# Kernel tuning notes

Measured on AMD Instinct MI355X. Metric: run time of the kernel, lower is better.

Reference implementation:

```python
import jax, jax.numpy as jnp
import numpy as np

K_VALUES = (2, 4, 8)  # sorted k_values from init


def setup_inputs() -> dict:
    key = jax.random.key(0)
    ks = jax.random.split(key, 6)
    B, T, D, H = 16, 2048, 512, 64
    nk = len(K_VALUES)
    # columns: (E, Pt, eta, phi) -- E,Pt positive, eta in [-3,3], phi in [-pi,pi]
    u = jax.random.uniform(ks[0], (B, T, 4), jnp.float32)
    tokens_cont = u * jnp.array([100.0, 50.0, 6.0, 6.2832], jnp.float32) + jnp.array([1.0, 1.0, -3.0, -3.1416], jnp.float32)
    lengths = jax.random.randint(ks[1], (B,), T // 2, T + 1)
    mask = jnp.arange(T)[None, :] < lengths[:, None]  # [B,T] True=valid
    W1 = jax.random.normal(ks[2], (nk, H), jnp.float32) / np.sqrt(nk).astype(np.float32)
    b1 = jax.random.normal(ks[3], (H,), jnp.float32) * 0.01
    W2 = jax.random.normal(ks[4], (H, D), jnp.float32) / np.sqrt(H).astype(np.float32)
    b2 = jax.random.normal(ks[5], (D,), jnp.float32) * 0.01
    return dict(tokens_cont=tokens_cont, mask=mask, W1=W1, b1=b1, W2=W2, b2=b2)


def reference(tokens_cont, mask, W1, b1, W2, b2):
    B, T, _ = tokens_cont.shape
    E, Pt, eta, phi = (tokens_cont[..., i] for i in range(4))
    px = Pt * jnp.cos(phi)
    py = Pt * jnp.sin(phi)
    pz = Pt * jnp.sinh(jnp.clip(eta, -20.0, 20.0))
    P = jnp.stack([E, px, py, pz], axis=-1)  # [B,T,4] four-momentum
    metric = jnp.array([1.0, -1.0, -1.0, -1.0], P.dtype)
    # Lorentz dot: E_i E_j - px_i px_j - py_i py_j - pz_i pz_j -> [B,T,T]
    dot = jnp.einsum('btc,bsc->bts', P * metric, P)
    dot = jnp.where(mask[:, None, :], dot, -jnp.inf)  # exclude padding friends
    max_k = min(max(K_VALUES), T)
    _, topk_idx = jax.lax.top_k(dot, max_k)  # [B,T,max_k]
    Pf = P[jnp.arange(B)[:, None, None], topk_idx]  # gather friends [B,T,max_k,4]
    cum = jnp.cumsum(Pf, axis=2)  # prefix sums over sorted friends
    masses = []
    maskf = mask.astype(P.dtype)
    for k in K_VALUES:
        ps = cum[:, :, min(k, max_k) - 1, :]  # [B,T,4] summed 4-momentum of top-k group
        m2 = ps[..., 0] ** 2 - jnp.sum(ps[..., 1:] ** 2, axis=-1)
        m2 = jnp.maximum(m2, 0.0) * maskf
        masses.append(jnp.sqrt(m2 + 1e-8))
    mass = jnp.stack(masses, axis=-1)  # [B,T,n_k]
    h = jax.nn.gelu(mass @ W1 + b1, approximate=False)  # torch GELU = exact erf
    return h @ W2 + b2  # [B,T,model_dim]
```

## Files before the change

kernel.cpp:

```cpp
#include <hip/hip_runtime.h>
#include <hip/hip_bf16.h>
#include <math.h>

#define NB 16
#define NT 2048
#define ND 512
#define NH 64

typedef __attribute__((ext_vector_type(8))) short short8;
typedef __attribute__((ext_vector_type(4))) float float4v;

__device__ __forceinline__ bool mask_is_bytes(const int* m) {
    return m[0] == 0x01010101;
}
__device__ __forceinline__ bool mask_at(const int* m, bool bytes, int i) {
    if (bytes) return ((const unsigned char*)m)[i] != 0;
    return m[i] != 0;
}

__device__ __forceinline__ float dot4(float4 a, float4 p) {
    float d = a.x * p.x;
    d = __builtin_fmaf(a.y, p.y, d);
    d = __builtin_fmaf(a.z, p.z, d);
    d = __builtin_fmaf(a.w, p.w, d);
    return d;
}

__device__ __forceinline__ unsigned short f2bf(float x) {
    unsigned int u = __float_as_uint(x);
    u += 0x7fffu + ((u >> 16) & 1u);
    return (unsigned short)(u >> 16);
}

#define CHAIN8(v0,v1,v2,v3,v4,v5,v6,v7,d) do {                 \
    float n0 = fmaxf(v0, d);                                    \
    float n1 = __builtin_amdgcn_fmed3f(d, v0, v1);              \
    float n2 = __builtin_amdgcn_fmed3f(d, v1, v2);              \
    float n3 = __builtin_amdgcn_fmed3f(d, v2, v3);              \
    float n4 = __builtin_amdgcn_fmed3f(d, v3, v4);              \
    float n5 = __builtin_amdgcn_fmed3f(d, v4, v5);              \
    float n6 = __builtin_amdgcn_fmed3f(d, v5, v6);              \
    float n7 = __builtin_amdgcn_fmed3f(d, v6, v7);              \
    v0 = n0; v1 = n1; v2 = n2; v3 = n3;                         \
    v4 = n4; v5 = n5; v6 = n6; v7 = n7;                         \
} while (0)

__global__ void __launch_bounds__(256) prep_kernel(
        const float* __restrict__ tok, const int* __restrict__ mask,
        const float* __restrict__ W2, unsigned short* __restrict__ W2t,
        float4* __restrict__ Pg) {
    int i = blockIdx.x * 256 + threadIdx.x;
    if (i < ND * NH) {
        int n = i & (ND - 1), k = i >> 9;
        W2t[n * NH + k] = f2bf(W2[k * ND + n]);
    } else {
        int j = i - ND * NH;
        const bool mb = mask_is_bytes(mask);
        float4 tv = ((const float4*)tok)[j];
        bool m = mask_at(mask, mb, j);
        float E = tv.x, Pt = tv.y, eta = tv.z, phi = tv.w;
        float px = Pt * cosf(phi);
        float py = Pt * sinf(phi);
        float pz = Pt * sinhf(fminf(fmaxf(eta, -20.f), 20.f));
        Pg[j] = m ? make_float4(E, px, py, pz)
                  : make_float4(-1e30f, 0.f, 0.f, 0.f);
    }
}

#define VTA(w2, j, l)  scratch[((w2) * 8 + (j)) * 64 + (l)]
#define VTB(w2, j, l)  scratch[4096 + ((w2) * 8 + (j)) * 64 + (l)]
#define PSA(w2, c, l)  scratch[((w2) * 12 + (c)) * 64 + (l)]
#define PSB(w2, c, l)  scratch[6144 + ((w2) * 12 + (c)) * 64 + (l)]

__global__ void __launch_bounds__(512) fused_topk_mass_mlp_kernel(
        const int* __restrict__ mask,
        const float* __restrict__ W1,
        const float* __restrict__ b1,
        const unsigned short* __restrict__ W2t,
        const float* __restrict__ b2,
        const float4* __restrict__ Pg,
        float* __restrict__ out) {
    __shared__ __align__(16) unsigned char smem_raw[32768 + 49152];
    __shared__ int wcnt[8];
    float* Plds            = (float*)smem_raw;
    float* scratch         = (float*)(smem_raw + 32768);
    unsigned short (*hs)[88] = (unsigned short(*)[88])smem_raw;
    float (*mass_s)[128]   = (float(*)[128])(smem_raw + 12288);

    const int b    = blockIdx.y;
    const int x    = blockIdx.x;
    const int tA   = 64 * x;
    const int tB   = 1024 + 64 * x;
    const int tid  = threadIdx.x;
    const int lane = tid & 63;
    const int w    = tid >> 6;
    const bool mb  = mask_is_bytes(mask);
    const float NEGBIG = -3.402823466e38f;
    const float MZ = sqrtf(1e-8f);

    int cnt = 0;
    const float4* __restrict__ Pb = Pg + (size_t)b * NT;
#pragma unroll
    for (int it = 0; it < 4; ++it) {
        int i = tid + it * 512;
        *(float4*)&Plds[i * 4] = Pb[i];
        cnt += (int)__popcll(__ballot(mask_at(mask, mb, b * NT + i)));
    }
    if (lane == 0) wcnt[w] = cnt;
    __syncthreads();

    int L = 0;
#pragma unroll
    for (int j = 0; j < 8; ++j) L += wcnt[j];
    const int C    = (L + 7) >> 3;
    const int sBeg = w * C;
    const int sEnd = min(sBeg + C, L);
    const bool hasB = tB < L;

    float4 pA = *(const float4*)&Plds[(tA + lane) * 4];
    float4 pBq = *(const float4*)&Plds[(tB + lane) * 4];
    float4 aA = make_float4(pA.x, -pA.y, -pA.z, -pA.w);
    float4 aB = make_float4(pBq.x, -pBq.y, -pBq.z, -pBq.w);

    float vA0 = NEGBIG, vA1 = NEGBIG, vA2 = NEGBIG, vA3 = NEGBIG;
    float vA4 = NEGBIG, vA5 = NEGBIG, vA6 = NEGBIG, vA7 = NEGBIG;
    float vB0 = NEGBIG, vB1 = NEGBIG, vB2 = NEGBIG, vB3 = NEGBIG;
    float vB4 = NEGBIG, vB5 = NEGBIG, vB6 = NEGBIG, vB7 = NEGBIG;

    if (hasB) {
#pragma unroll 4
        for (int s = sBeg; s < sEnd; ++s) {
            float4 ps = *(const float4*)&Plds[s * 4];
            float dA = dot4(aA, ps);
            float dB = dot4(aB, ps);
            CHAIN8(vA0, vA1, vA2, vA3, vA4, vA5, vA6, vA7, dA);
            CHAIN8(vB0, vB1, vB2, vB3, vB4, vB5, vB6, vB7, dB);
        }
    } else {
#pragma unroll 4
        for (int s = sBeg; s < sEnd; ++s) {
            float4 ps = *(const float4*)&Plds[s * 4];
            float dA = dot4(aA, ps);
            CHAIN8(vA0, vA1, vA2, vA3, vA4, vA5, vA6, vA7, dA);
        }
    }
    VTA(w, 0, lane) = vA0; VTA(w, 1, lane) = vA1;
    VTA(w, 2, lane) = vA2; VTA(w, 3, lane) = vA3;
    VTA(w, 4, lane) = vA4; VTA(w, 5, lane) = vA5;
    VTA(w, 6, lane) = vA6; VTA(w, 7, lane) = vA7;
    if (hasB) {
        VTB(w, 0, lane) = vB0; VTB(w, 1, lane) = vB1;
        VTB(w, 2, lane) = vB2; VTB(w, 3, lane) = vB3;
        VTB(w, 4, lane) = vB4; VTB(w, 5, lane) = vB5;
        VTB(w, 6, lane) = vB6; VTB(w, 7, lane) = vB7;
    }
    __syncthreads();

    float thA2, thA4, thA8;
    {
        float m0 = NEGBIG, m1 = NEGBIG, m2_ = NEGBIG, m3 = NEGBIG;
        float m4 = NEGBIG, m5 = NEGBIG, m6 = NEGBIG, m7 = NEGBIG;
#pragma unroll
        for (int w2 = 0; w2 < 8; ++w2)
#pragma unroll
            for (int j = 0; j < 8; ++j) {
                float d = VTA(w2, j, lane);
                CHAIN8(m0, m1, m2_, m3, m4, m5, m6, m7, d);
            }
        thA2 = m1; thA4 = m3; thA8 = m7;
    }
    float thB2 = 0.f, thB4 = 0.f, thB8 = 0.f;
    if (hasB) {
        float m0 = NEGBIG, m1 = NEGBIG, m2_ = NEGBIG, m3 = NEGBIG;
        float m4 = NEGBIG, m5 = NEGBIG, m6 = NEGBIG, m7 = NEGBIG;
#pragma unroll
        for (int w2 = 0; w2 < 8; ++w2)
#pragma unroll
            for (int j = 0; j < 8; ++j) {
                float d = VTB(w2, j, lane);
                CHAIN8(m0, m1, m2_, m3, m4, m5, m6, m7, d);
            }
        thB2 = m1; thB4 = m3; thB8 = m7;
    }
    __syncthreads();

    {
        float a2x = 0.f, a2y = 0.f, a2z = 0.f, a2w = 0.f;
        float a4x = 0.f, a4y = 0.f, a4z = 0.f, a4w = 0.f;
        float a8x = 0.f, a8y = 0.f, a8z = 0.f, a8w = 0.f;
        float b2x = 0.f, b2y = 0.f, b2z = 0.f, b2w = 0.f;
        float b4x = 0.f, b4y = 0.f, b4z = 0.f, b4w = 0.f;
        float b8x = 0.f, b8y = 0.f, b8z = 0.f, b8w = 0.f;
        if (hasB) {
#pragma unroll 4
            for (int s = sBeg; s < sEnd; ++s) {
                float4 ps = *(const float4*)&Plds[s * 4];
                float dA = dot4(aA, ps);
                float dB = dot4(aB, ps);
                if (dA >= thA8) {
                    a8x += ps.x; a8y += ps.y; a8z += ps.z; a8w += ps.w;
                    if (dA >= thA4) {
                        a4x += ps.x; a4y += ps.y; a4z += ps.z; a4w += ps.w;
                        if (dA >= thA2) {
                            a2x += ps.x; a2y += ps.y; a2z += ps.z; a2w += ps.w;
                        }
                    }
                }
                if (dB >= thB8) {
                    b8x += ps.x; b8y += ps.y; b8z += ps.z; b8w += ps.w;
                    if (dB >= thB4) {
                        b4x += ps.x; b4y += ps.y; b4z += ps.z; b4w += ps.w;
                        if (dB >= thB2) {
                            b2x += ps.x; b2y += ps.y; b2z += ps.z; b2w += ps.w;
                        }
                    }
                }
            }
        } else {
#pragma unroll 4
            for (int s = sBeg; s < sEnd; ++s) {
                float4 ps = *(const float4*)&Plds[s * 4];
                float dA = dot4(aA, ps);
                if (dA >= thA8) {
                    a8x += ps.x; a8y += ps.y; a8z += ps.z; a8w += ps.w;
                    if (dA >= thA4) {
                        a4x += ps.x; a4y += ps.y; a4z += ps.z; a4w += ps.w;
                        if (dA >= thA2) {
                            a2x += ps.x; a2y += ps.y; a2z += ps.z; a2w += ps.w;
                        }
                    }
                }
            }
        }
        PSA(w, 0, lane) = a2x;  PSA(w, 1, lane) = a2y;
        PSA(w, 2, lane) = a2z;  PSA(w, 3, lane) = a2w;
        PSA(w, 4, lane) = a4x;  PSA(w, 5, lane) = a4y;
        PSA(w, 6, lane) = a4z;  PSA(w, 7, lane) = a4w;
        PSA(w, 8, lane) = a8x;  PSA(w, 9, lane) = a8y;
        PSA(w, 10, lane) = a8z; PSA(w, 11, lane) = a8w;
        if (hasB) {
            PSB(w, 0, lane) = b2x;  PSB(w, 1, lane) = b2y;
            PSB(w, 2, lane) = b2z;  PSB(w, 3, lane) = b2w;
            PSB(w, 4, lane) = b4x;  PSB(w, 5, lane) = b4y;
            PSB(w, 6, lane) = b4z;  PSB(w, 7, lane) = b4w;
            PSB(w, 8, lane) = b8x;  PSB(w, 9, lane) = b8y;
            PSB(w, 10, lane) = b8z; PSB(w, 11, lane) = b8w;
        }
    }
    __syncthreads();

    {
        auto massf = [](float sx, float sy, float sz, float sw) -> float {
            float q = sx * sx;
            q = __builtin_fmaf(-sy, sy, q);
            q = __builtin_fmaf(-sz, sz, q);
            q = __builtin_fmaf(-sw, sw, q);
            q = fmaxf(q, 0.f);
            return sqrtf(q + 1e-8f);
        };
        if (w == 0) {
            float tot[12];
#pragma unroll
            for (int c = 0; c < 12; ++c) {
                float acc = 0.f;
#pragma unroll
                for (int w2 = 0; w2 < 8; ++w2) acc += PSA(w2, c, lane);
                tot[c] = acc;
            }
            mass_s[0][lane] = massf(tot[0], tot[1], tot[2], tot[3]);
            mass_s[1][lane] = massf(tot[4], tot[5], tot[6], tot[7]);
            mass_s[2][lane] = massf(tot[8], tot[9], tot[10], tot[11]);
        } else if (w == 1) {
            if (hasB) {
                float tot[12];
#pragma unroll
                for (int c = 0; c < 12; ++c) {
                    float acc = 0.f;
#pragma unroll
                    for (int w2 = 0; w2 < 8; ++w2) acc += PSB(w2, c, lane);
                    tot[c] = acc;
                }
                const bool maskt = (tB + lane) < L;
                mass_s[0][64 + lane] = maskt ? massf(tot[0], tot[1], tot[2], tot[3]) : MZ;
                mass_s[1][64 + lane] = maskt ? massf(tot[4], tot[5], tot[6], tot[7]) : MZ;
                mass_s[2][64 + lane] = maskt ? massf(tot[8], tot[9], tot[10], tot[11]) : MZ;
            } else {
                mass_s[0][64 + lane] = MZ;
                mass_s[1][64 + lane] = MZ;
                mass_s[2][64 + lane] = MZ;
            }
        }
    }
    __syncthreads();

    const int col   = lane & 15;
    const int quad  = lane >> 4;
    const int mhalf = w >> 2;
    const int nBase = (w & 3) * 128;

#pragma unroll 1
    for (int m = 0; m < 2; ++m) {
        if (m) __syncthreads();

        {
            float q0 = mass_s[0][m * 64 + lane];
            float q1 = mass_s[1][m * 64 + lane];
            float q2 = mass_s[2][m * 64 + lane];
            unsigned short hv[8];
#pragma unroll
            for (int j = 0; j < 8; ++j) {
                int hh = w * 8 + j;
                float pre = b1[hh];
                pre = __builtin_fmaf(q0, W1[hh], pre);
                pre = __builtin_fmaf(q1, W1[NH + hh], pre);
                pre = __builtin_fmaf(q2, W1[2 * NH + hh], pre);
                float g = 0.5f * pre * (1.0f + erff(pre * 0.70710678118654752f));
                hv[j] = f2bf(g);
            }
            *(short8*)&hs[lane][w * 8] = *(const short8*)hv;
        }
        __syncthreads();

        short8 afrag[2][2];
#pragma unroll
        for (int mt = 0; mt < 2; ++mt)
#pragma unroll
            for (int ks = 0; ks < 2; ++ks)
                afrag[mt][ks] = *(const short8*)&hs[mhalf * 32 + mt * 16 + col][ks * 32 + quad * 8];

        float4v acc[2][8];
#pragma unroll
        for (int mt = 0; mt < 2; ++mt)
#pragma unroll
            for (int nt = 0; nt < 8; ++nt)
                acc[mt][nt] = (float4v)(0.f);

#pragma unroll
        for (int nt = 0; nt < 8; ++nt) {
            const unsigned short* wp = W2t + (nBase + nt * 16 + col) * NH + quad * 8;
            short8 bf0 = *(const short8*)(wp);
            short8 bf1 = *(const short8*)(wp + 32);
            acc[0][nt] = __builtin_amdgcn_mfma_f32_16x16x32_bf16(afrag[0][0], bf0, acc[0][nt], 0, 0, 0);
            acc[1][nt] = __builtin_amdgcn_mfma_f32_16x16x32_bf16(afrag[1][0], bf0, acc[1][nt], 0, 0, 0);
            acc[0][nt] = __builtin_amdgcn_mfma_f32_16x16x32_bf16(afrag[0][1], bf1, acc[0][nt], 0, 0, 0);
            acc[1][nt] = __builtin_amdgcn_mfma_f32_16x16x32_bf16(afrag[1][1], bf1, acc[1][nt], 0, 0, 0);
        }

        const int tileBase = b * NT + (m ? tB : tA);
#pragma unroll
        for (int nt = 0; nt < 8; ++nt) {
            float bias = b2[nBase + nt * 16 + col];
#pragma unroll
            for (int mt = 0; mt < 2; ++mt) {
                int mRow = tileBase + mhalf * 32 + mt * 16 + quad * 4;
                size_t base = (size_t)mRow * ND + nBase + nt * 16 + col;
#pragma unroll
                for (int r = 0; r < 4; ++r) {
                    out[base + (size_t)r * ND] = acc[mt][nt][r] + bias;
                }
            }
        }
    }
}

extern "C" void kernel_launch(void* const* d_in, const int* in_sizes, int n_in,
                              void* d_out, int out_size, void* d_ws, size_t ws_size,
                              hipStream_t stream) {
    const float* tok  = (const float*)d_in[0];
    const int*   mask = (const int*)d_in[1];
    const float* W1   = (const float*)d_in[2];
    const float* b1   = (const float*)d_in[3];
    const float* W2   = (const float*)d_in[4];
    const float* b2   = (const float*)d_in[5];
    float*       out  = (float*)d_out;

    unsigned short* W2t = (unsigned short*)d_ws;
    float4*         Pg  = (float4*)((char*)d_ws + 0x10000);

    prep_kernel<<<dim3((ND * NH + NB * NT) / 256), dim3(256), 0, stream>>>(
        tok, mask, W2, W2t, Pg);

    dim3 gB(NT / 128, NB);
    fused_topk_mass_mlp_kernel<<<gB, dim3(512), 0, stream>>>(
        mask, W1, b1, W2t, b2, Pg, out);
}
```

Baseline: 144.7 us.

## Double block to 1024 threads, split friend scan across 16 waves, parallelize MLP halves

Raises the fused kernel block size from 512 to 1024 threads, so the per-batch friend scan is divided among 16 waves instead of 8. Each wave therefore walks half as many candidates. Threshold merging moves to two dedicated waves that publish their results through shared memory. The two 64-token MLP halves now run concurrently on separate wave groups with separate h buffers, instead of in a sequential loop. In exchange, the merge over partial top-8 lists and partial sums becomes longer, there are more registers per block to fit, and occupancy may drop to one block per CU.

Measured after the change: 137.7 us. 1.05x faster.

```diff
diff --git a/kernel.cpp b/kernel.cpp
--- a/kernel.cpp
+++ b/kernel.cpp
@@ -6,6 +6,7 @@
 #define NT 2048
 #define ND 512
 #define NH 64
+#define NW 16
 
 typedef __attribute__((ext_vector_type(8))) short short8;
 typedef __attribute__((ext_vector_type(4))) float float4v;
@@ -67,12 +68,12 @@
     }
 }
 
-#define VTA(w2, j, l)  scratch[((w2) * 8 + (j)) * 64 + (l)]
-#define VTB(w2, j, l)  scratch[4096 + ((w2) * 8 + (j)) * 64 + (l)]
-#define PSA(w2, c, l)  scratch[((w2) * 12 + (c)) * 64 + (l)]
-#define PSB(w2, c, l)  scratch[6144 + ((w2) * 12 + (c)) * 64 + (l)]
-
-__global__ void __launch_bounds__(512) fused_topk_mass_mlp_kernel(
+#define VTA(w2, j, l)  S[ 8192 + ((w2) * 8 + (j)) * 64 + (l)]
+#define VTB(w2, j, l)  S[16384 + ((w2) * 8 + (j)) * 64 + (l)]
+#define PSA(w2, c, l)  S[ 8192 + ((w2) * 12 + (c)) * 64 + (l)]
+#define PSB(w2, c, l)  S[20480 + ((w2) * 12 + (c)) * 64 + (l)]
+
+__global__ void __launch_bounds__(1024) fused_topk_mass_mlp_kernel(
         const int* __restrict__ mask,
         const float* __restrict__ W1,
         const float* __restrict__ b1,
@@ -80,12 +81,14 @@
         const float* __restrict__ b2,
         const float4* __restrict__ Pg,
         float* __restrict__ out) {
-    __shared__ __align__(16) unsigned char smem_raw[32768 + 49152];
-    __shared__ int wcnt[8];
-    float* Plds            = (float*)smem_raw;
-    float* scratch         = (float*)(smem_raw + 32768);
-    unsigned short (*hs)[88] = (unsigned short(*)[88])smem_raw;
-    float (*mass_s)[128]   = (float(*)[128])(smem_raw + 12288);
+    __shared__ __align__(16) float S[32768];
+    __shared__ float thS[6][64];
+    __shared__ int wcnt[NW];
+
+    float* Plds = S;
+    unsigned short (*hsA)[88] = (unsigned short(*)[88])S;
+    unsigned short (*hsB)[88] = (unsigned short(*)[88])(S + 2816);
+    float (*mass_s)[128]      = (float(*)[128])(S + 5632);
 
     const int b    = blockIdx.y;
     const int x    = blockIdx.x;
@@ -101,8 +104,8 @@
     int cnt = 0;
     const float4* __restrict__ Pb = Pg + (size_t)b * NT;
 #pragma unroll
-    for (int it = 0; it < 4; ++it) {
-        int i = tid + it * 512;
+    for (int it = 0; it < 2; ++it) {
+        int i = tid + it * 1024;
         *(float4*)&Plds[i * 4] = Pb[i];
         cnt += (int)__popcll(__ballot(mask_at(mask, mb, b * NT + i)));
     }
@@ -111,13 +114,13 @@
 
     int L = 0;
 #pragma unroll
-    for (int j = 0; j < 8; ++j) L += wcnt[j];
-    const int C    = (L + 7) >> 3;
+    for (int j = 0; j < NW; ++j) L += wcnt[j];
+    const int C    = (L + NW - 1) / NW;
     const int sBeg = w * C;
     const int sEnd = min(sBeg + C, L);
     const bool hasB = tB < L;
 
-    float4 pA = *(const float4*)&Plds[(tA + lane) * 4];
+    float4 pA  = *(const float4*)&Plds[(tA + lane) * 4];
     float4 pBq = *(const float4*)&Plds[(tB + lane) * 4];
     float4 aA = make_float4(pA.x, -pA.y, -pA.z, -pA.w);
     float4 aB = make_float4(pBq.x, -pBq.y, -pBq.z, -pBq.w);
@@ -156,33 +159,35 @@
     }
     __syncthreads();
 
-    float thA2, thA4, thA8;
-    {
+    if (w == 0) {
         float m0 = NEGBIG, m1 = NEGBIG, m2_ = NEGBIG, m3 = NEGBIG;
         float m4 = NEGBIG, m5 = NEGBIG, m6 = NEGBIG, m7 = NEGBIG;
 #pragma unroll
-        for (int w2 = 0; w2 < 8; ++w2)
+        for (int w2 = 0; w2 < NW; ++w2)
 #pragma unroll
             for (int j = 0; j < 8; ++j) {
                 float d = VTA(w2, j, lane);
                 CHAIN8(m0, m1, m2_, m3, m4, m5, m6, m7, d);
             }
-        thA2 = m1; thA4 = m3; thA8 = m7;
-    }
-    float thB2 = 0.f, thB4 = 0.f, thB8 = 0.f;
-    if (hasB) {
+        thS[0][lane] = m1; thS[1][lane] = m3; thS[2][lane] = m7;
+    } else if (w == 1 && hasB) {
         float m0 = NEGBIG, m1 = NEGBIG, m2_ = NEGBIG, m3 = NEGBIG;
         float m4 = NEGBIG, m5 = NEGBIG, m6 = NEGBIG, m7 = NEGBIG;
 #pragma unroll
-        for (int w2 = 0; w2 < 8; ++w2)
+        for (int w2 = 0; w2 < NW; ++w2)
 #pragma unroll
             for (int j = 0; j < 8; ++j) {
                 float d = VTB(w2, j, lane);
                 CHAIN8(m0, m1, m2_, m3, m4, m5, m6, m7, d);
             }
-        thB2 = m1; thB4 = m3; thB8 = m7;
-    }
-    __syncthreads();
+        thS[3][lane] = m1; thS[4][lane] = m3; thS[5][lane] = m7;
+    }
+    __syncthreads();
+
+    const float thA2 = thS[0][lane], thA4 = thS[1][lane], thA8 = thS[2][lane];
+    const float thB2 = hasB ? thS[3][lane] : 0.f;
+    const float thB4 = hasB ? thS[4][lane] : 0.f;
+    const float thB8 = hasB ? thS[5][lane] : 0.f;
 
     {
         float a2x = 0.f, a2y = 0.f, a2z = 0.f, a2w = 0.f;
@@ -264,7 +269,7 @@
             for (int c = 0; c < 12; ++c) {
                 float acc = 0.f;
 #pragma unroll
-                for (int w2 = 0; w2 < 8; ++w2) acc += PSA(w2, c, lane);
+                for (int w2 = 0; w2 < NW; ++w2) acc += PSA(w2, c, lane);
                 tot[c] = acc;
             }
             mass_s[0][lane] = massf(tot[0], tot[1], tot[2], tot[3]);
@@ -277,7 +282,7 @@
                 for (int c = 0; c < 12; ++c) {
                     float acc = 0.f;
 #pragma unroll
-                    for (int w2 = 0; w2 < 8; ++w2) acc += PSB(w2, c, lane);
+                    for (int w2 = 0; w2 < NW; ++w2) acc += PSB(w2, c, lane);
                     tot[c] = acc;
                 }
                 const bool maskt = (tB + lane) < L;
@@ -293,71 +298,69 @@
     }
     __syncthreads();
 
+    const int m     = w >> 3;
+    const int wl    = w & 7;
     const int col   = lane & 15;
     const int quad  = lane >> 4;
-    const int mhalf = w >> 2;
-    const int nBase = (w & 3) * 128;
-
-#pragma unroll 1
-    for (int m = 0; m < 2; ++m) {
-        if (m) __syncthreads();
-
-        {
-            float q0 = mass_s[0][m * 64 + lane];
-            float q1 = mass_s[1][m * 64 + lane];
-            float q2 = mass_s[2][m * 64 + lane];
-            unsigned short hv[8];
-#pragma unroll
-            for (int j = 0; j < 8; ++j) {
-                int hh = w * 8 + j;
-                float pre = b1[hh];
-                pre = __builtin_fmaf(q0, W1[hh], pre);
-                pre = __builtin_fmaf(q1, W1[NH + hh], pre);
-                pre = __builtin_fmaf(q2, W1[2 * NH + hh], pre);
-                float g = 0.5f * pre * (1.0f + erff(pre * 0.70710678118654752f));
-                hv[j] = f2bf(g);
-            }
-            *(short8*)&hs[lane][w * 8] = *(const short8*)hv;
-        }
-        __syncthreads();
-
-        short8 afrag[2][2];
-#pragma unroll
-        for (int mt = 0; mt < 2; ++mt)
-#pragma unroll
-            for (int ks = 0; ks < 2; ++ks)
-                afrag[mt][ks] = *(const short8*)&hs[mhalf * 32 + mt * 16 + col][ks * 32 + quad * 8];
-
-        float4v acc[2][8];
-#pragma unroll
-        for (int mt = 0; mt < 2; ++mt)
-#pragma unroll
-            for (int nt = 0; nt < 8; ++nt)
-                acc[mt][nt] = (float4v)(0.f);
-
-#pragma unroll
-        for (int nt = 0; nt < 8; ++nt) {
-            const unsigned short* wp = W2t + (nBase + nt * 16 + col) * NH + quad * 8;
-            short8 bf0 = *(const short8*)(wp);
-            short8 bf1 = *(const short8*)(wp + 32);
-            acc[0][nt] = __builtin_amdgcn_mfma_f32_16x16x32_bf16(afrag[0][0], bf0, acc[0][nt], 0, 0, 0);
-            acc[1][nt] = __builtin_amdgcn_mfma_f32_16x16x32_bf16(afrag[1][0], bf0, acc[1][nt], 0, 0, 0);
-            acc[0][nt] = __builtin_amdgcn_mfma_f32_16x16x32_bf16(afrag[0][1], bf1, acc[0][nt], 0, 0, 0);
-            acc[1][nt] = __builtin_amdgcn_mfma_f32_16x16x32_bf16(afrag[1][1], bf1, acc[1][nt], 0, 0, 0);
-        }
-
-        const int tileBase = b * NT + (m ? tB : tA);
-#pragma unroll
-        for (int nt = 0; nt < 8; ++nt) {
-            float bias = b2[nBase + nt * 16 + col];
-#pragma unroll
-            for (int mt = 0; mt < 2; ++mt) {
-                int mRow = tileBase + mhalf * 32 + mt * 16 + quad * 4;
-                size_t base = (size_t)mRow * ND + nBase + nt * 16 + col;
-#pragma unroll
-                for (int r = 0; r < 4; ++r) {
-                    out[base + (size_t)r * ND] = acc[mt][nt][r] + bias;
-                }
+    const int mhalf = wl >> 2;
+    const int nBase = (wl & 3) * 128;
+    unsigned short (*hsm)[88] = m ? hsB : hsA;
+
+    {
+        float q0 = mass_s[0][m * 64 + lane];
+        float q1 = mass_s[1][m * 64 + lane];
+        float q2 = mass_s[2][m * 64 + lane];
+        unsigned short hv[8];
+#pragma unroll
+        for (int j = 0; j < 8; ++j) {
+            int hh = wl * 8 + j;
+            float pre = b1[hh];
+            pre = __builtin_fmaf(q0, W1[hh], pre);
+            pre = __builtin_fmaf(q1, W1[NH + hh], pre);
+            pre = __builtin_fmaf(q2, W1[2 * NH + hh], pre);
+            float g = 0.5f * pre * (1.0f + erff(pre * 0.70710678118654752f));
+            hv[j] = f2bf(g);
+        }
+        *(short8*)&hsm[lane][wl * 8] = *(const short8*)hv;
+    }
+    __syncthreads();
+
+    short8 afrag[2][2];
+#pragma unroll
+    for (int mt = 0; mt < 2; ++mt)
+#pragma unroll
+        for (int ks = 0; ks < 2; ++ks)
+            afrag[mt][ks] = *(const short8*)&hsm[mhalf * 32 + mt * 16 + col][ks * 32 + quad * 8];
+
+    float4v acc[2][8];
+#pragma unroll
+    for (int mt = 0; mt < 2; ++mt)
+#pragma unroll
+        for (int nt = 0; nt < 8; ++nt)
+            acc[mt][nt] = (float4v)(0.f);
+
+#pragma unroll
+    for (int nt = 0; nt < 8; ++nt) {
+        const unsigned short* wp = W2t + (nBase + nt * 16 + col) * NH + quad * 8;
+        short8 bf0 = *(const short8*)(wp);
+        short8 bf1 = *(const short8*)(wp + 32);
+        acc[0][nt] = __builtin_amdgcn_mfma_f32_16x16x32_bf16(afrag[0][0], bf0, acc[0][nt], 0, 0, 0);
+        acc[1][nt] = __builtin_amdgcn_mfma_f32_16x16x32_bf16(afrag[1][0], bf0, acc[1][nt], 0, 0, 0);
+        acc[0][nt] = __builtin_amdgcn_mfma_f32_16x16x32_bf16(afrag[0][1], bf1, acc[0][nt], 0, 0, 0);
+        acc[1][nt] = __builtin_amdgcn_mfma_f32_16x16x32_bf16(afrag[1][1], bf1, acc[1][nt], 0, 0, 0);
+    }
+
+    const int tileBase = b * NT + (m ? tB : tA);
+#pragma unroll
+    for (int nt = 0; nt < 8; ++nt) {
+        float bias = b2[nBase + nt * 16 + col];
+#pragma unroll
+        for (int mt = 0; mt < 2; ++mt) {
+            int mRow = tileBase + mhalf * 32 + mt * 16 + quad * 4;
+            size_t base = (size_t)mRow * ND + nBase + nt * 16 + col;
+#pragma unroll
+            for (int r = 0; r < 4; ++r) {
+                out[base + (size_t)r * ND] = acc[mt][nt][r] + bias;
             }
         }
     }
@@ -381,6 +384,6 @@
         tok, mask, W2, W2t, Pg);
 
     dim3 gB(NT / 128, NB);
-    fused_topk_mass_mlp_kernel<<<gB, dim3(512), 0, stream>>>(
+    fused_topk_mass_mlp_kernel<<<gB, dim3(1024), 0, stream>>>(
         mask, W1, b1, W2t, b2, Pg, out);
 }
```
